# Performance work log

Hardware: AMD Instinct MI355X
Metric: run time of the kernel (lower is better)

## Reference

```python
import jax, jax.numpy as jnp
import numpy as np

# sizes
A, P, E = 2000, 20000, 200000
MUL0, MUL1 = 128, 64            # 128x0e + 64x1o
DIM = MUL0 + 3 * MUL1            # 320
NBASIS, FC_HID = 10, 100
WNUM = MUL0 + MUL0 + MUL1 + MUL1 # 384 tp weights per edge
MID0 = MUL0 + MUL1               # 192 scalar channels in irreps_mid
NUM_NEIGHBORS = 10.0


def setup_inputs() -> dict:
    key = jax.random.key(0)
    ks = jax.random.split(key, 20)
    # edge attr = spherical harmonics lmax=1 (component norm): [1, sqrt(3)*unit_vec]
    vec = jax.random.normal(ks[0], (E, 3))
    unit = vec / jnp.linalg.norm(vec, axis=1, keepdims=True)
    edge_attr = jnp.concatenate([jnp.ones((E, 1)), jnp.sqrt(3.0) * unit], axis=1)
    return {
        "sender_input": jax.random.normal(ks[1], (A, DIM)),
        "sender_attr": jnp.ones((A, 1)),
        "receiver_input": jax.random.normal(ks[2], (P, DIM)),
        "receiver_attr": jnp.ones((P, 1)),
        "edge_src": jax.random.randint(ks[3], (E,), 0, A, dtype=jnp.int32),
        "edge_dst": jax.random.randint(ks[4], (E,), 0, P, dtype=jnp.int32),
        "edge_attr": edge_attr,
        "edge_scalars": jax.random.normal(ks[5], (E, NBASIS)),  # normalized radial basis
        # FC net (no bias, e3nn FullyConnectedNet style)
        "fc_w1": jax.random.normal(ks[6], (NBASIS, FC_HID)),
        "fc_w2": jax.random.normal(ks[7], (FC_HID, WNUM)),
        # lin1: FCTP(sender, 0e, sender) -> per-l linear on multiplicities
        "lin1_w0": jax.random.normal(ks[8], (MUL0, MUL0)),
        "lin1_w1": jax.random.normal(ks[9], (MUL1, MUL1)),
        # sc: FCTP(receiver, 0e, output)
        "sc_w0": jax.random.normal(ks[10], (MUL0, MUL0)),
        "sc_w1": jax.random.normal(ks[11], (MUL1, MUL1)),
        # lin2: FCTP(mid, 0e, output)
        "lin2_w0": jax.random.normal(ks[12], (MID0, MUL0)),
        "lin2_w1": jax.random.normal(ks[13], (MID0, MUL1)),
        # lin3: FCTP(mid, 0e, 0e) -> only scalar part contributes
        "lin3_w": jax.random.normal(ks[14], (MID0, 1)),
    }


def reference(sender_input, sender_attr, receiver_input, receiver_attr,
              edge_src, edge_dst, edge_attr, edge_scalars,
              fc_w1, fc_w2, lin1_w0, lin1_w1, sc_w0, sc_w1,
              lin2_w0, lin2_w1, lin3_w):
    f32 = jnp.float32
    # per-edge tensor-product weights from radial MLP (silu, fan-in normalized)
    h = jax.nn.silu(edge_scalars @ fc_w1 * (1.0 / np.sqrt(NBASIS)))
    weight = h @ fc_w2 * (1.0 / np.sqrt(FC_HID))                      # [E, 384]

    # self-connection on receivers (scalar attr -> per-l linear)
    r_in = receiver_input * receiver_attr
    sc0 = r_in[:, :MUL0] @ sc_w0 * (1.0 / np.sqrt(MUL0))              # [P,128]
    sc1 = jnp.einsum('pum,uv->pvm', r_in[:, MUL0:].reshape(-1, MUL1, 3), sc_w1) * (1.0 / np.sqrt(MUL1))
    sc_out = jnp.concatenate([sc0, sc1.reshape(-1, 3 * MUL1)], axis=1)  # [P,320]

    # lin1 on senders
    s_in = sender_input * sender_attr
    s0 = s_in[:, :MUL0] @ lin1_w0 * (1.0 / np.sqrt(MUL0))             # [A,128]
    s1 = jnp.einsum('aum,uv->avm', s_in[:, MUL0:].reshape(-1, MUL1, 3), lin1_w1) * (1.0 / np.sqrt(MUL1))

    # gather sender features to edges
    g0 = s0[edge_src]                                                  # [E,128]
    g1 = s1[edge_src]                                                  # [E,64,3]
    sh0 = edge_attr[:, :1]                                             # [E,1]
    sh1 = edge_attr[:, 1:]                                             # [E,3]

    # weighted 'uvu' tensor product paths (instruction order)
    w0 = weight[:, :MUL0]
    w1 = weight[:, MUL0:2 * MUL0]
    w2 = weight[:, 2 * MUL0:2 * MUL0 + MUL1]
    w3 = weight[:, 2 * MUL0 + MUL1:]
    out0a = w0 * g0 * sh0                                              # 0e x 0e -> 0e  [E,128]
    out1a = (w1 * g0)[:, :, None] * sh1[:, None, :]                    # 0e x 1o -> 1o  [E,128,3]
    out1b = w2[:, :, None] * g1 * sh0[:, None, :]                      # 1o x 0e -> 1o  [E,64,3]
    out0b = w3 * jnp.einsum('eum,em->eu', g1, sh1) * (1.0 / np.sqrt(3.0))  # 1o x 1o -> 0e [E,64]
    # irreps_mid sorted: 128x0e + 64x0e + 128x1o + 64x1o  -> 768 dims
    edge_feat = jnp.concatenate([out0a, out0b,
                                 out1a.reshape(-1, 3 * MUL0),
                                 out1b.reshape(-1, 3 * MUL1)], axis=1)

    # scatter-add to receivers
    r = jax.ops.segment_sum(edge_feat, edge_dst, num_segments=receiver_input.shape[0])
    r = r * (1.0 / np.sqrt(NUM_NEIGHBORS))                             # [P,768]
    r = r * receiver_attr
    r0 = r[:, :MID0]
    r1 = r[:, MID0:].reshape(-1, MID0, 3)

    conv0 = r0 @ lin2_w0 * (1.0 / np.sqrt(MID0))                        # [P,128]
    conv1 = jnp.einsum('pum,uv->pvm', r1, lin2_w1) * (1.0 / np.sqrt(MID0))
    conv_out = jnp.concatenate([conv0, conv1.reshape(-1, 3 * MUL1)], axis=1)

    angle = 0.1 * (r0 @ lin3_w * (1.0 / np.sqrt(MID0)))                 # [P,1]
    # sc.output_mask is all-ones here (every output irrep has a path)
    return jnp.cos(angle) * sc_out + jnp.sin(angle) * conv_out          # [P,320]
```

## Files before the change

### kernel.cpp

```cpp
#include <hip/hip_runtime.h>
#include <hip/hip_bf16.h>
#include <math.h>

#define A_N    2000
#define P_N    20000
#define PPAD   20032
#define E_N    200000
#define MUL0   128
#define MUL1   64
#define DIM    320
#define NBASIS 10
#define FC_HID 100
#define WNUM   384
#define MID0   192
#define OV     128

#define RS10   0.31622776601683794f
#define RS100  0.1f
#define RS128  0.08838834764831845f
#define RS64   0.125f
#define RS192  0.07216878364870323f
#define RS3    0.5773502691896258f
#define RSNEI  0.31622776601683794f

typedef __bf16 bf16x8 __attribute__((ext_vector_type(8)));
typedef float  f32x4  __attribute__((ext_vector_type(4)));

__device__ __forceinline__ float bflo(unsigned u) { return __uint_as_float(u << 16); }
__device__ __forceinline__ float bfhi(unsigned u) { return __uint_as_float(u & 0xffff0000u); }

__global__ __launch_bounds__(320) void sender_kernel(
    const float* __restrict__ sender_input, const float* __restrict__ sender_attr,
    const float* __restrict__ lin1_w0, const float* __restrict__ lin1_w1,
    __bf16* __restrict__ s_pack)
{
    __shared__ float sin_s[DIM];
    const int a = blockIdx.x;
    const int t = threadIdx.x;
    const float attr = sender_attr[a];
    sin_s[t] = sender_input[(size_t)a * DIM + t] * attr;
    __syncthreads();
    __bf16* row = s_pack + (size_t)a * 384;
    if (t < MUL0) {
        float acc = 0.f;
        for (int u = 0; u < MUL0; ++u)
            acc = fmaf(sin_s[u], lin1_w0[u * MUL0 + t], acc);
        row[(t & 63) * 6 + (t >> 6)] = (__bf16)(acc * RS128);
    } else {
        const int idx = t - MUL0;
        const int v = idx / 3, m = idx - 3 * v;
        float acc = 0.f;
        for (int u = 0; u < MUL1; ++u)
            acc = fmaf(sin_s[MUL0 + 3 * u + m], lin1_w1[u * MUL1 + v], acc);
        row[v * 6 + 2 + m] = (__bf16)(acc * RS64);
    }
    if (t < 64) row[t * 6 + 5] = (__bf16)0.f;
}

__global__ __launch_bounds__(256) void hist_kernel(
    const int* __restrict__ edge_dst, int* __restrict__ counts)
{
    const int e = blockIdx.x * 256 + threadIdx.x;
    if (e < E_N) atomicAdd(&counts[edge_dst[e]], 1);
}

__global__ __launch_bounds__(1024) void scan_kernel(
    const int* __restrict__ counts, int* __restrict__ head)
{
    __shared__ int part[1024];
    const int t = threadIdx.x;
    const int base = t * 20;
    int c[20];
    int s = 0;
    #pragma unroll
    for (int i = 0; i < 20; ++i) {
        const int p = base + i;
        c[i] = (p < P_N) ? counts[p] : 0;
        s += c[i];
    }
    part[t] = s;
    __syncthreads();
    for (int off = 1; off < 1024; off <<= 1) {
        const int v = (t >= off) ? part[t - off] : 0;
        __syncthreads();
        part[t] += v;
        __syncthreads();
    }
    int run = (t > 0) ? part[t - 1] : 0;
    #pragma unroll
    for (int i = 0; i < 20; ++i) {
        const int p = base + i;
        if (p < P_N) { head[p] = run; run += c[i]; }
    }
}

__global__ __launch_bounds__(256) void scatter_kernel(
    const int* __restrict__ edge_dst, const int* __restrict__ edge_src,
    const float4* __restrict__ edge_attr4,
    int* __restrict__ head, int* __restrict__ sorted,
    int* __restrict__ src_sorted, float4* __restrict__ attr_sorted)
{
    const int e = blockIdx.x * 256 + threadIdx.x;
    if (e < E_N) {
        const int pos = atomicAdd(&head[edge_dst[e]], 1);
        sorted[pos]      = e;
        src_sorted[pos]  = edge_src[e];
        attr_sorted[pos] = edge_attr4[e];
    }
}

__global__ __launch_bounds__(256) void pack_w2_kernel(
    const float* __restrict__ fc_w2, __bf16* __restrict__ w2p)
{
    const int tid  = blockIdx.x * 256 + threadIdx.x;
    const int lane = tid & 63;
    const int g    = (tid >> 6) & 3;
    const int n    = tid >> 8;
    const int col  = n * 16 + (lane & 15);
    const int kb   = g * 32 + 8 * (lane >> 4);
    bf16x8 v;
    #pragma unroll
    for (int i = 0; i < 8; ++i) {
        const int k = kb + i;
        v[i] = (__bf16)((k < FC_HID) ? fc_w2[k * WNUM + col] * RS100 : 0.f);
    }
    ((bf16x8*)w2p)[tid] = v;
}

__global__ __launch_bounds__(256) void pack_kernel(
    const float* __restrict__ src, __bf16* __restrict__ dst,
    int K, int KG, int N, float scale)
{
    const int tid  = blockIdx.x * 256 + threadIdx.x;
    const int lane = tid & 63;
    const int fi   = tid >> 6;
    const int g    = fi % KG;
    const int n    = fi / KG;
    const int col  = n * 16 + (lane & 15);
    const int kb   = g * 32 + 8 * (lane >> 4);
    bf16x8 v;
    #pragma unroll
    for (int i = 0; i < 8; ++i) {
        const int k = kb + i;
        v[i] = (__bf16)((k < K) ? src[(size_t)k * N + col] * scale : 0.f);
    }
    ((bf16x8*)dst)[tid] = v;
}

__global__ __launch_bounds__(256) void mlp_gemm_chunk_kernel(
    const int* __restrict__ sorted,
    const float* __restrict__ edge_scalars,
    const float* __restrict__ fc_w1, const __bf16* __restrict__ w2p,
    __bf16* __restrict__ wbuf, int cLo)
{
    __shared__ float  fc1s[NBASIS * 128];
    __shared__ float  es_s[64][11];
    __shared__ int    eid_s[64];
    __shared__ __attribute__((aligned(16))) __bf16 hstage[32 * 384];

    const int tid   = threadIdx.x;
    const int wave  = tid >> 6;
    const int lane  = tid & 63;
    const int pbase = blockIdx.x * 64;

    if (tid < 64) {
        int gi = cLo + pbase + tid;
        if (gi >= E_N) gi = E_N - 1;
        eid_s[tid] = sorted[gi];
    }
    for (int f = tid; f < NBASIS * FC_HID; f += 256) {
        const int i = f / FC_HID, k = f - i * FC_HID;
        fc1s[i * 128 + (k ^ ((k & 96) >> 3))] = fc_w1[f];
    }
    __syncthreads();

    for (int f = tid; f < 64 * NBASIS; f += 256) {
        const int e = f / NBASIS, i = f - e * NBASIS;
        es_s[e][i] = edge_scalars[(size_t)eid_s[e] * NBASIS + i];
    }
    __syncthreads();

    __bf16* h_lds = hstage;
    {
        const int e  = tid >> 2;
        const int k0 = (tid & 3) * 32;
        const int kx = (tid & 3) * 4;
        float es[NBASIS];
        #pragma unroll
        for (int i = 0; i < NBASIS; ++i) es[i] = es_s[e][i];
        #pragma unroll
        for (int o = 0; o < 4; ++o) {
            bf16x8 hv;
            #pragma unroll
            for (int j = 0; j < 8; ++j) {
                const int r = o * 8 + j;
                const int k = k0 + r;
                float x = 0.f;
                if (k < FC_HID) {
                    const int ks = k0 + (r ^ kx);
                    #pragma unroll
                    for (int i = 0; i < NBASIS; ++i)
                        x = fmaf(es[i], fc1s[i * 128 + ks], x);
                    x *= RS10;
                    x = x / (1.f + __expf(-x));
                }
                hv[j] = (__bf16)x;
            }
            const int idx = (e * 128 + k0 + o * 8) ^ ((e & 7) << 3);
            *(bf16x8*)&h_lds[idx] = hv;
        }
    }
    __syncthreads();

    bf16x8 a[4][4];
    const int arow = lane & 15, ag = lane >> 4;
    #pragma unroll
    for (int mt = 0; mt < 4; ++mt) {
        const int e = mt * 16 + arow;
        #pragma unroll
        for (int g = 0; g < 4; ++g) {
            const int idx = (e * 128 + g * 32 + ag * 8) ^ ((e & 7) << 3);
            a[mt][g] = *(const bf16x8*)&h_lds[idx];
        }
    }

    const bf16x8* w2v = (const bf16x8*)w2p;
    const int row0 = 4 * (lane >> 4), col16 = lane & 15;

    #pragma unroll
    for (int half = 0; half < 2; ++half) {
        __syncthreads();
        for (int nt = 0; nt < 6; ++nt) {
            const int ntile = wave * 6 + nt;
            bf16x8 b[4];
            #pragma unroll
            for (int g = 0; g < 4; ++g)
                b[g] = w2v[(ntile * 4 + g) * 64 + lane];
            const int L = ntile * 16 + col16;
            const int slot = (L & 63) * 6 + (L >> 6);
            #pragma unroll
            for (int mtl = 0; mtl < 2; ++mtl) {
                const int mt = half * 2 + mtl;
                f32x4 acc = {0.f, 0.f, 0.f, 0.f};
                #pragma unroll
                for (int g = 0; g < 4; ++g)
                    acc = __builtin_amdgcn_mfma_f32_16x16x32_bf16(a[mt][g], b[g],
                                                                  acc, 0, 0, 0);
                __bf16* sp = &hstage[(mtl * 16 + row0) * 384 + slot];
                #pragma unroll
                for (int j = 0; j < 4; ++j)
                    sp[j * 384] = (__bf16)acc[j];
            }
        }
        __syncthreads();
        const int srow = tid >> 3;
        const float4* sp4 = (const float4*)&hstage[srow * 384 + (tid & 7) * 48];
        float4* gp4 = (float4*)((char*)wbuf
                      + (size_t)(pbase + half * 32 + srow) * 768
                      + (size_t)(tid & 7) * 96);
        #pragma unroll
        for (int q = 0; q < 6; ++q) gp4[q] = sp4[q];
    }
}

__global__ __launch_bounds__(256) void gather_kernel(
    const int* __restrict__ head, const int* __restrict__ counts,
    const int* __restrict__ src_sorted, const float4* __restrict__ attr_sorted,
    const __bf16* __restrict__ wbuf, const __bf16* __restrict__ s_pack,
    const float* __restrict__ receiver_input, const float* __restrict__ receiver_attr,
    const float* __restrict__ lin3_w,
    __bf16* __restrict__ rbuf, __bf16* __restrict__ rinp,
    float* __restrict__ cs_arr, float* __restrict__ sn_arr,
    int cLo, int cHi)
{
    __shared__ int sel_s[4];
    const int tid  = threadIdx.x;
    const int wave = tid >> 6;
    const int lane = tid & 63;
    const int p = blockIdx.x * 4 + wave;

    const int cnt   = counts[p];
    const int start = head[p] - cnt;
    const int sel   = (start >= cLo) & (start < cHi);

    if (lane == 0) sel_s[wave] = sel;
    __syncthreads();
    if ((sel_s[0] | sel_s[1] | sel_s[2] | sel_s[3]) == 0) return;
    if (!sel) return;

    float acc[12];
    #pragma unroll
    for (int i = 0; i < 12; ++i) acc[i] = 0.f;

    #pragma unroll 2
    for (int i = 0; i < cnt; ++i) {
        const int pos = start + i;
        const unsigned* wq = (const unsigned*)((const char*)wbuf
                             + (size_t)(pos - cLo) * 768 + lane * 12);
        const int    src = src_sorted[pos];
        const float4 ea  = attr_sorted[pos];
        const unsigned* sq = (const unsigned*)((const char*)s_pack
                             + (size_t)src * 768 + lane * 12);
        const unsigned w01 = wq[0], w23 = wq[1], w45 = wq[2];
        const unsigned s01 = sq[0], s23 = sq[1], s45 = sq[2];

        const float sh0 = ea.x, sh1x = ea.y, sh1y = ea.z, sh1z = ea.w;
        const float w0a = bflo(w01), w0b = bfhi(w01);
        const float w1a = bflo(w23), w1b = bfhi(w23);
        const float w2v = bflo(w45), w3v = bfhi(w45);
        const float g0a = bflo(s01), g0b = bfhi(s01);
        const float g1x = bflo(s23), g1y = bfhi(s23), g1z = bflo(s45);

        acc[0] = fmaf(w0a * g0a, sh0, acc[0]);
        acc[1] = fmaf(w0b * g0b, sh0, acc[1]);
        const float dotg = fmaf(g1x, sh1x, fmaf(g1y, sh1y, g1z * sh1z)) * RS3;
        acc[2] = fmaf(w3v, dotg, acc[2]);
        const float p1a = w1a * g0a, p1b = w1b * g0b;
        acc[3] = fmaf(p1a, sh1x, acc[3]);
        acc[4] = fmaf(p1a, sh1y, acc[4]);
        acc[5] = fmaf(p1a, sh1z, acc[5]);
        acc[6] = fmaf(p1b, sh1x, acc[6]);
        acc[7] = fmaf(p1b, sh1y, acc[7]);
        acc[8] = fmaf(p1b, sh1z, acc[8]);
        const float q = w2v * sh0;
        acc[9]  = fmaf(q, g1x, acc[9]);
        acc[10] = fmaf(q, g1y, acc[10]);
        acc[11] = fmaf(q, g1z, acc[11]);
    }

    const float rattr = receiver_attr[p];
    const float rfac  = RSNEI * rattr;
    const float v0 = acc[0] * rfac, v1 = acc[1] * rfac, v2 = acc[2] * rfac;

    float part = v0 * lin3_w[lane] + v1 * lin3_w[64 + lane] + v2 * lin3_w[128 + lane];
    #pragma unroll
    for (int off = 1; off < 64; off <<= 1) part += __shfl_xor(part, off);
    if (lane == 0) {
        const float a = part * 0.1f * RS192;
        cs_arr[p] = __cosf(a);
        sn_arr[p] = __sinf(a);
    }

    __bf16* rb = rbuf + (size_t)p * 768;
    rb[lane]       = (__bf16)v0;
    rb[64 + lane]  = (__bf16)v1;
    rb[128 + lane] = (__bf16)v2;
    #pragma unroll
    for (int m = 0; m < 3; ++m) {
        __bf16* r1 = rb + 192 + m * 192;
        r1[lane]        = (__bf16)(acc[3 + m] * rfac);
        r1[64 + lane]   = (__bf16)(acc[6 + m] * rfac);
        r1[128 + lane]  = (__bf16)(acc[9 + m] * rfac);
    }

    __bf16* rp = rinp + (size_t)p * 320;
    #pragma unroll
    for (int q = 0; q < 5; ++q) {
        const int t = q * 64 + lane;
        const float val = receiver_input[(size_t)p * DIM + t] * rattr;
        int pos;
        if (t < 128) pos = t;
        else { const int idx = t - 128; const int u = idx / 3, m = idx - 3 * u;
               pos = 128 + m * 64 + u; }
        rp[pos] = (__bf16)val;
    }
}

__global__ __launch_bounds__(256) void out_transform_kernel(
    const __bf16* __restrict__ rbuf, const __bf16* __restrict__ rinp,
    const __bf16* __restrict__ scw0p, const __bf16* __restrict__ l2w0p,
    const __bf16* __restrict__ scw1p, const __bf16* __restrict__ l2w1p,
    const float* __restrict__ cs_arr, const float* __restrict__ sn_arr,
    float* __restrict__ out)
{
    const int wave = threadIdx.x >> 6, lane = threadIdx.x & 63;
    const int pw0 = blockIdx.x * 64 + wave * 16;
    const int arow = lane & 15, ag = lane >> 4;
    const int crow0 = 4 * (lane >> 4), ccol = lane & 15;

    const size_t riRow = (size_t)(pw0 + arow) * 320;
    const size_t rbRow = (size_t)(pw0 + arow) * 768;

    float cs[4], sn[4];
    #pragma unroll
    for (int j = 0; j < 4; ++j) {
        cs[j] = cs_arr[pw0 + crow0 + j];
        sn[j] = sn_arr[pw0 + crow0 + j];
    }

    {
        bf16x8 ain[4], arr[6];
        #pragma unroll
        for (int g = 0; g < 4; ++g)
            ain[g] = *(const bf16x8*)&rinp[riRow + g * 32 + ag * 8];
        #pragma unroll
        for (int g = 0; g < 6; ++g)
            arr[g] = *(const bf16x8*)&rbuf[rbRow + g * 32 + ag * 8];
        #pragma unroll
        for (int nt = 0; nt < 8; ++nt) {
            f32x4 asc = {0.f, 0.f, 0.f, 0.f}, acv = {0.f, 0.f, 0.f, 0.f};
            #pragma unroll
            for (int g = 0; g < 4; ++g)
                asc = __builtin_amdgcn_mfma_f32_16x16x32_bf16(
                    ain[g], ((const bf16x8*)scw0p)[(nt * 4 + g) * 64 + lane], asc, 0, 0, 0);
            #pragma unroll
            for (int g = 0; g < 6; ++g)
                acv = __builtin_amdgcn_mfma_f32_16x16x32_bf16(
                    arr[g], ((const bf16x8*)l2w0p)[(nt * 6 + g) * 64 + lane], acv, 0, 0, 0);
            #pragma unroll
            for (int j = 0; j < 4; ++j) {
                const int row = pw0 + crow0 + j;
                if (row < P_N)
                    out[(size_t)row * DIM + nt * 16 + ccol] =
                        cs[j] * asc[j] + sn[j] * acv[j];
            }
        }
    }
    #pragma unroll
    for (int m = 0; m < 3; ++m) {
        bf16x8 ain1[2], arr1[6];
        #pragma unroll
        for (int g = 0; g < 2; ++g)
            ain1[g] = *(const bf16x8*)&rinp[riRow + 128 + m * 64 + g * 32 + ag * 8];
        #pragma unroll
        for (int g = 0; g < 6; ++g)
            arr1[g] = *(const bf16x8*)&rbuf[rbRow + 192 + m * 192 + g * 32 + ag * 8];
        #pragma unroll
        for (int vt = 0; vt < 4; ++vt) {
            f32x4 asc = {0.f, 0.f, 0.f, 0.f}, acv = {0.f, 0.f, 0.f, 0.f};
            #pragma unroll
            for (int g = 0; g < 2; ++g)
                asc = __builtin_amdgcn_mfma_f32_16x16x32_bf16(
                    ain1[g], ((const bf16x8*)scw1p)[(vt * 2 + g) * 64 + lane], asc, 0, 0, 0);
            #pragma unroll
            for (int g = 0; g < 6; ++g)
                acv = __builtin_amdgcn_mfma_f32_16x16x32_bf16(
                    arr1[g], ((const bf16x8*)l2w1p)[(vt * 6 + g) * 64 + lane], acv, 0, 0, 0);
            #pragma unroll
            for (int j = 0; j < 4; ++j) {
                const int row = pw0 + crow0 + j;
                if (row < P_N) {
                    const int v = vt * 16 + ccol;
                    out[(size_t)row * DIM + MUL0 + 3 * v + m] =
                        cs[j] * asc[j] + sn[j] * acv[j];
                }
            }
        }
    }
}

extern "C" void kernel_launch(void* const* d_in, const int* in_sizes, int n_in,
                              void* d_out, int out_size, void* d_ws, size_t ws_size,
                              hipStream_t stream)
{
    const float* sender_input   = (const float*)d_in[0];
    const float* sender_attr    = (const float*)d_in[1];
    const float* receiver_input = (const float*)d_in[2];
    const float* receiver_attr  = (const float*)d_in[3];
    const int*   edge_src       = (const int*)  d_in[4];
    const int*   edge_dst       = (const int*)  d_in[5];
    const float* edge_attr      = (const float*)d_in[6];
    const float* edge_scalars   = (const float*)d_in[7];
    const float* fc_w1          = (const float*)d_in[8];
    const float* fc_w2          = (const float*)d_in[9];
    const float* lin1_w0        = (const float*)d_in[10];
    const float* lin1_w1        = (const float*)d_in[11];
    const float* sc_w0          = (const float*)d_in[12];
    const float* sc_w1          = (const float*)d_in[13];
    const float* lin2_w0        = (const float*)d_in[14];
    const float* lin2_w1        = (const float*)d_in[15];
    const float* lin3_w         = (const float*)d_in[16];
    float* out = (float*)d_out;

    char* wsb = (char*)d_ws;
    float4* attr_sorted = (float4*)wsb;
    __bf16* s_pack = (__bf16*)(wsb + (size_t)E_N * 16);
    __bf16* w2p    = s_pack + (size_t)A_N * 384;
    __bf16* scw0p  = w2p   + 24 * 4 * 64 * 8;
    __bf16* l2w0p  = scw0p +  8 * 4 * 64 * 8;
    __bf16* scw1p  = l2w0p +  8 * 6 * 64 * 8;
    __bf16* l2w1p  = scw1p +  4 * 2 * 64 * 8;
    __bf16* rbuf   = l2w1p +  4 * 6 * 64 * 8;
    __bf16* rinp   = rbuf + (size_t)PPAD * 768;
    float*  cs_arr = (float*)(rinp + (size_t)PPAD * 320);
    float*  sn_arr = cs_arr + PPAD;
    int* counts     = (int*)(sn_arr + PPAD);
    int* head       = counts + P_N;
    int* sorted     = head + P_N;
    int* src_sorted = sorted + E_N;
    __bf16* wbuf    = (__bf16*)(src_sorted + E_N);
    const size_t fixedB = (size_t)((char*)wbuf - wsb);

    long long maxpos = (long long)((ws_size - fixedB) / 768);
    long long cc = (maxpos - OV - 64) & ~63LL;
    int cchunk = (cc > E_N) ? E_N : (int)cc;

    sender_kernel<<<A_N, 320, 0, stream>>>(sender_input, sender_attr,
                                           lin1_w0, lin1_w1, s_pack);
    pack_w2_kernel<<<24, 256, 0, stream>>>(fc_w2, w2p);
    pack_kernel<<< 8, 256, 0, stream>>>(sc_w0,   scw0p, 128, 4, 128, RS128);
    pack_kernel<<<12, 256, 0, stream>>>(lin2_w0, l2w0p, 192, 6, 128, RS192);
    pack_kernel<<< 2, 256, 0, stream>>>(sc_w1,   scw1p, 64,  2, 64,  RS64);
    pack_kernel<<< 6, 256, 0, stream>>>(lin2_w1, l2w1p, 192, 6, 64,  RS192);

    hipMemsetAsync(counts, 0, P_N * sizeof(int), stream);
    hist_kernel<<<(E_N + 255) / 256, 256, 0, stream>>>(edge_dst, counts);
    scan_kernel<<<1, 1024, 0, stream>>>(counts, head);
    scatter_kernel<<<(E_N + 255) / 256, 256, 0, stream>>>(
        edge_dst, edge_src, (const float4*)edge_attr,
        head, sorted, src_sorted, attr_sorted);

    for (int cLo = 0; cLo < E_N; cLo += cchunk) {
        int nPos = E_N - cLo;
        if (nPos > cchunk + OV) nPos = cchunk + OV;
        const int cHi = (cLo + cchunk >= E_N) ? (E_N + 1) : (cLo + cchunk);
        mlp_gemm_chunk_kernel<<<(nPos + 63) / 64, 256, 0, stream>>>(
            sorted, edge_scalars, fc_w1, w2p, wbuf, cLo);
        gather_kernel<<<P_N / 4, 256, 0, stream>>>(
            head, counts, src_sorted, attr_sorted, wbuf, s_pack,
            receiver_input, receiver_attr, lin3_w,
            rbuf, rinp, cs_arr, sn_arr, cLo, cHi);
    }

    out_transform_kernel<<<(P_N + 63) / 64, 256, 0, stream>>>(
        rbuf, rinp, scw0p, l2w0p, scw1p, l2w1p, cs_arr, sn_arr, out);
}
```

Baseline: 245.0 us.

## Prefetch gather loads, pad LDS stride, merge MLP prologue, split out-transform blocks

The gather loop now software-pipelines its loads: the next edge's weights, sender features and attributes, and the source index two edges ahead, are fetched while the current edge is accumulated, to hide global-load latency. The MLP kernel pads the staging stride to 392 to reduce LDS bank conflicts and unrolls the n-tile loop by two. It also fuses the sorted-index lookup into the edge-scalar load, removing one barrier. The output transform launches twice as many blocks, splitting scalar and vector outputs into separate blocks for more parallelism, at the cost of some duplicated cs/sn loads and more register pressure from prefetching.

```diff
diff --git a/kernel.cpp b/kernel.cpp
--- a/kernel.cpp
+++ b/kernel.cpp
@@ -14,6 +14,7 @@
 #define WNUM   384
 #define MID0   192
 #define OV     128
+#define SSTRIDE 392
 
 #define RS10   0.31622776601683794f
 #define RS100  0.1f
@@ -155,28 +156,22 @@
 {
     __shared__ float  fc1s[NBASIS * 128];
     __shared__ float  es_s[64][11];
-    __shared__ int    eid_s[64];
-    __shared__ __attribute__((aligned(16))) __bf16 hstage[32 * 384];
+    __shared__ __attribute__((aligned(16))) __bf16 hstage[32 * SSTRIDE];
 
     const int tid   = threadIdx.x;
     const int wave  = tid >> 6;
     const int lane  = tid & 63;
     const int pbase = blockIdx.x * 64;
 
-    if (tid < 64) {
-        int gi = cLo + pbase + tid;
+    for (int f = tid; f < 64 * NBASIS; f += 256) {
+        const int e = f / NBASIS, i = f - e * NBASIS;
+        int gi = cLo + pbase + e;
         if (gi >= E_N) gi = E_N - 1;
-        eid_s[tid] = sorted[gi];
+        es_s[e][i] = edge_scalars[(size_t)sorted[gi] * NBASIS + i];
     }
     for (int f = tid; f < NBASIS * FC_HID; f += 256) {
         const int i = f / FC_HID, k = f - i * FC_HID;
         fc1s[i * 128 + (k ^ ((k & 96) >> 3))] = fc_w1[f];
-    }
-    __syncthreads();
-
-    for (int f = tid; f < 64 * NBASIS; f += 256) {
-        const int e = f / NBASIS, i = f - e * NBASIS;
-        es_s[e][i] = edge_scalars[(size_t)eid_s[e] * NBASIS + i];
     }
     __syncthreads();
 
@@ -230,6 +225,7 @@
     #pragma unroll
     for (int half = 0; half < 2; ++half) {
         __syncthreads();
+        #pragma unroll 2
         for (int nt = 0; nt < 6; ++nt) {
             const int ntile = wave * 6 + nt;
             bf16x8 b[4];
@@ -246,15 +242,15 @@
                 for (int g = 0; g < 4; ++g)
                     acc = __builtin_amdgcn_mfma_f32_16x16x32_bf16(a[mt][g], b[g],
                                                                   acc, 0, 0, 0);
-                __bf16* sp = &hstage[(mtl * 16 + row0) * 384 + slot];
+                __bf16* sp = &hstage[(mtl * 16 + row0) * SSTRIDE + slot];
                 #pragma unroll
                 for (int j = 0; j < 4; ++j)
-                    sp[j * 384] = (__bf16)acc[j];
+                    sp[j * SSTRIDE] = (__bf16)acc[j];
             }
         }
         __syncthreads();
         const int srow = tid >> 3;
-        const float4* sp4 = (const float4*)&hstage[srow * 384 + (tid & 7) * 48];
+        const float4* sp4 = (const float4*)&hstage[srow * SSTRIDE + (tid & 7) * 48];
         float4* gp4 = (float4*)((char*)wbuf
                       + (size_t)(pbase + half * 32 + srow) * 768
                       + (size_t)(tid & 7) * 96);
@@ -292,40 +288,56 @@
     #pragma unroll
     for (int i = 0; i < 12; ++i) acc[i] = 0.f;
 
-    #pragma unroll 2
-    for (int i = 0; i < cnt; ++i) {
-        const int pos = start + i;
-        const unsigned* wq = (const unsigned*)((const char*)wbuf
-                             + (size_t)(pos - cLo) * 768 + lane * 12);
-        const int    src = src_sorted[pos];
-        const float4 ea  = attr_sorted[pos];
-        const unsigned* sq = (const unsigned*)((const char*)s_pack
-                             + (size_t)src * 768 + lane * 12);
-        const unsigned w01 = wq[0], w23 = wq[1], w45 = wq[2];
-        const unsigned s01 = sq[0], s23 = sq[1], s45 = sq[2];
-
-        const float sh0 = ea.x, sh1x = ea.y, sh1y = ea.z, sh1z = ea.w;
-        const float w0a = bflo(w01), w0b = bfhi(w01);
-        const float w1a = bflo(w23), w1b = bfhi(w23);
-        const float w2v = bflo(w45), w3v = bfhi(w45);
-        const float g0a = bflo(s01), g0b = bfhi(s01);
-        const float g1x = bflo(s23), g1y = bfhi(s23), g1z = bflo(s45);
-
-        acc[0] = fmaf(w0a * g0a, sh0, acc[0]);
-        acc[1] = fmaf(w0b * g0b, sh0, acc[1]);
-        const float dotg = fmaf(g1x, sh1x, fmaf(g1y, sh1y, g1z * sh1z)) * RS3;
-        acc[2] = fmaf(w3v, dotg, acc[2]);
-        const float p1a = w1a * g0a, p1b = w1b * g0b;
-        acc[3] = fmaf(p1a, sh1x, acc[3]);
-        acc[4] = fmaf(p1a, sh1y, acc[4]);
-        acc[5] = fmaf(p1a, sh1z, acc[5]);
-        acc[6] = fmaf(p1b, sh1x, acc[6]);
-        acc[7] = fmaf(p1b, sh1y, acc[7]);
-        acc[8] = fmaf(p1b, sh1z, acc[8]);
-        const float q = w2v * sh0;
-        acc[9]  = fmaf(q, g1x, acc[9]);
-        acc[10] = fmaf(q, g1y, acc[10]);
-        acc[11] = fmaf(q, g1z, acc[11]);
+    if (cnt > 0) {
+        const char* wb  = (const char*)wbuf;
+        const char* spk = (const char*)s_pack;
+        const int last = start + cnt - 1;
+
+        const unsigned* wq0 = (const unsigned*)(wb + (size_t)(start - cLo) * 768 + lane * 12);
+        unsigned cw0 = wq0[0], cw1 = wq0[1], cw2 = wq0[2];
+        float4 cea = attr_sorted[start];
+        int csrc = src_sorted[start];
+        const unsigned* sq0 = (const unsigned*)(spk + (size_t)csrc * 768 + lane * 12);
+        unsigned cs0 = sq0[0], cs1 = sq0[1], cs2 = sq0[2];
+        int nsrc = src_sorted[(start + 1 <= last) ? start + 1 : last];
+
+        for (int i = 0; i < cnt; ++i) {
+            const int pn = (start + i + 1 <= last) ? start + i + 1 : last;
+            const unsigned* wqn = (const unsigned*)(wb + (size_t)(pn - cLo) * 768 + lane * 12);
+            const unsigned nw0 = wqn[0], nw1 = wqn[1], nw2 = wqn[2];
+            const float4 nea = attr_sorted[pn];
+            const unsigned* sqn = (const unsigned*)(spk + (size_t)nsrc * 768 + lane * 12);
+            const unsigned ns0 = sqn[0], ns1 = sqn[1], ns2 = sqn[2];
+            int p2 = start + i + 2; if (p2 > last) p2 = last;
+            const int nnsrc = src_sorted[p2];
+
+            const float sh0 = cea.x, sh1x = cea.y, sh1y = cea.z, sh1z = cea.w;
+            const float w0a = bflo(cw0), w0b = bfhi(cw0);
+            const float w1a = bflo(cw1), w1b = bfhi(cw1);
+            const float w2v = bflo(cw2), w3v = bfhi(cw2);
+            const float g0a = bflo(cs0), g0b = bfhi(cs0);
+            const float g1x = bflo(cs1), g1y = bfhi(cs1), g1z = bflo(cs2);
+
+            acc[0] = fmaf(w0a * g0a, sh0, acc[0]);
+            acc[1] = fmaf(w0b * g0b, sh0, acc[1]);
+            const float dotg = fmaf(g1x, sh1x, fmaf(g1y, sh1y, g1z * sh1z)) * RS3;
+            acc[2] = fmaf(w3v, dotg, acc[2]);
+            const float p1a = w1a * g0a, p1b = w1b * g0b;
+            acc[3] = fmaf(p1a, sh1x, acc[3]);
+            acc[4] = fmaf(p1a, sh1y, acc[4]);
+            acc[5] = fmaf(p1a, sh1z, acc[5]);
+            acc[6] = fmaf(p1b, sh1x, acc[6]);
+            acc[7] = fmaf(p1b, sh1y, acc[7]);
+            acc[8] = fmaf(p1b, sh1z, acc[8]);
+            const float q = w2v * sh0;
+            acc[9]  = fmaf(q, g1x, acc[9]);
+            acc[10] = fmaf(q, g1y, acc[10]);
+            acc[11] = fmaf(q, g1z, acc[11]);
+
+            cw0 = nw0; cw1 = nw1; cw2 = nw2;
+            cs0 = ns0; cs1 = ns1; cs2 = ns2;
+            cea = nea; nsrc = nnsrc;
+        }
     }
 
     const float rattr = receiver_attr[p];
@@ -371,10 +383,12 @@
     const __bf16* __restrict__ scw0p, const __bf16* __restrict__ l2w0p,
     const __bf16* __restrict__ scw1p, const __bf16* __restrict__ l2w1p,
     const float* __restrict__ cs_arr, const float* __restrict__ sn_arr,
-    float* __restrict__ out)
+    float* __restrict__ out, int nbS)
 {
     const int wave = threadIdx.x >> 6, lane = threadIdx.x & 63;
-    const int pw0 = blockIdx.x * 64 + wave * 16;
+    const bool vec = (int)blockIdx.x >= nbS;
+    const int b = vec ? (int)blockIdx.x - nbS : (int)blockIdx.x;
+    const int pw0 = b * 64 + wave * 16;
     const int arow = lane & 15, ag = lane >> 4;
     const int crow0 = 4 * (lane >> 4), ccol = lane & 15;
 
@@ -388,7 +402,7 @@
         sn[j] = sn_arr[pw0 + crow0 + j];
     }
 
-    {
+    if (!vec) {
         bf16x8 ain[4], arr[6];
         #pragma unroll
         for (int g = 0; g < 4; ++g)
@@ -415,34 +429,35 @@
                         cs[j] * asc[j] + sn[j] * acv[j];
             }
         }
-    }
-    #pragma unroll
-    for (int m = 0; m < 3; ++m) {
-        bf16x8 ain1[2], arr1[6];
-        #pragma unroll
-        for (int g = 0; g < 2; ++g)
-            ain1[g] = *(const bf16x8*)&rinp[riRow + 128 + m * 64 + g * 32 + ag * 8];
-        #pragma unroll
-        for (int g = 0; g < 6; ++g)
-            arr1[g] = *(const bf16x8*)&rbuf[rbRow + 192 + m * 192 + g * 32 + ag * 8];
-        #pragma unroll
-        for (int vt = 0; vt < 4; ++vt) {
-            f32x4 asc = {0.f, 0.f, 0.f, 0.f}, acv = {0.f, 0.f, 0.f, 0.f};
+    } else {
+        #pragma unroll
+        for (int m = 0; m < 3; ++m) {
+            bf16x8 ain1[2], arr1[6];
             #pragma unroll
             for (int g = 0; g < 2; ++g)
-                asc = __builtin_amdgcn_mfma_f32_16x16x32_bf16(
-                    ain1[g], ((const bf16x8*)scw1p)[(vt * 2 + g) * 64 + lane], asc, 0, 0, 0);
+                ain1[g] = *(const bf16x8*)&rinp[riRow + 128 + m * 64 + g * 32 + ag * 8];
             #pragma unroll
             for (int g = 0; g < 6; ++g)
-                acv = __builtin_amdgcn_mfma_f32_16x16x32_bf16(
-                    arr1[g], ((const bf16x8*)l2w1p)[(vt * 6 + g) * 64 + lane], acv, 0, 0, 0);
-            #pragma unroll
-            for (int j = 0; j < 4; ++j) {
-                const int row = pw0 + crow0 + j;
-                if (row < P_N) {
-                    const int v = vt * 16 + ccol;
-                    out[(size_t)row * DIM + MUL0 + 3 * v + m] =
-                        cs[j] * asc[j] + sn[j] * acv[j];
+                arr1[g] = *(const bf16x8*)&rbuf[rbRow + 192 + m * 192 + g * 32 + ag * 8];
+            #pragma unroll
+            for (int vt = 0; vt < 4; ++vt) {
+                f32x4 asc = {0.f, 0.f, 0.f, 0.f}, acv = {0.f, 0.f, 0.f, 0.f};
+                #pragma unroll
+                for (int g = 0; g < 2; ++g)
+                    asc = __builtin_amdgcn_mfma_f32_16x16x32_bf16(
+                        ain1[g], ((const bf16x8*)scw1p)[(vt * 2 + g) * 64 + lane], asc, 0, 0, 0);
+                #pragma unroll
+                for (int g = 0; g < 6; ++g)
+                    acv = __builtin_amdgcn_mfma_f32_16x16x32_bf16(
+                        arr1[g], ((const bf16x8*)l2w1p)[(vt * 6 + g) * 64 + lane], acv, 0, 0, 0);
+                #pragma unroll
+                for (int j = 0; j < 4; ++j) {
+                    const int row = pw0 + crow0 + j;
+                    if (row < P_N) {
+                        const int v = vt * 16 + ccol;
+                        out[(size_t)row * DIM + MUL0 + 3 * v + m] =
+                            cs[j] * asc[j] + sn[j] * acv[j];
+                    }
                 }
             }
         }
@@ -522,6 +537,7 @@
             rbuf, rinp, cs_arr, sn_arr, cLo, cHi);
     }
 
-    out_transform_kernel<<<(P_N + 63) / 64, 256, 0, stream>>>(
-        rbuf, rinp, scw0p, l2w0p, scw1p, l2w1p, cs_arr, sn_arr, out);
-}
+    const int nbS = PPAD / 64;
+    out_transform_kernel<<<2 * nbS, 256, 0, stream>>>(
+        rbuf, rinp, scw0p, l2w0p, scw1p, l2w1p, cs_arr, sn_arr, out, nbS);
+}
```

Result: no change. 244.7 us (-0.1%).
